# Kernel tuning notes

Measured on AMD Instinct MI355X. Metric: run time of the kernel, lower is better.

Reference implementation:

```python
import jax, jax.numpy as jnp
import numpy as np

PS = 4        # bkg_patch_size
PD = 1        # replicate pad
UFSTRIDE = 2  # patch-extraction stride
STRIDE = 1    # correlation stride
SCALE = 10.0  # softmax_scale


def pad_edge(x):
    return jnp.pad(x, ((0, 0), (0, 0), (PD, PD), (PD, PD)), mode='edge')


def unfold(x, ps, stride):
    # x: (B,C,H,W) -> (B, L, C, ps, ps), row-major over patch grid (matches F.unfold)
    B, C, H, W = x.shape
    oh = (H - ps) // stride + 1
    ow = (W - ps) // stride + 1
    ih = jnp.arange(oh)[:, None] * stride + jnp.arange(ps)[None, :]  # (oh, ps)
    iw = jnp.arange(ow)[:, None] * stride + jnp.arange(ps)[None, :]  # (ow, ps)
    p = x[:, :, ih][:, :, :, :, iw]            # (B,C,oh,ps,ow,ps)
    p = p.transpose(0, 2, 4, 1, 3, 5)          # (B,oh,ow,C,ps,ps)
    return p.reshape(B, oh * ow, C, ps, ps)


def diag3(x):
    # conv2d with 3x3 identity kernel, padding=1: out[i,j] = in[i-1,j-1]+in[i,j]+in[i+1,j+1]
    B, one, N, M = x.shape
    xp = jnp.pad(x, ((0, 0), (0, 0), (1, 1), (1, 1)))
    return xp[:, :, 0:N, 0:M] + xp[:, :, 1:N + 1, 1:M + 1] + xp[:, :, 2:N + 2, 2:M + 2]


def setup_inputs() -> dict:
    key = jax.random.key(0)
    k1, k2, k3 = jax.random.split(key, 3)
    B, C, H, W = 4, 64, 64, 64
    f = jax.random.normal(k1, (B, C, H, W), dtype=jnp.float32)
    b = jax.random.normal(k2, (B, C, H, W), dtype=jnp.float32)
    mask = (jax.random.uniform(k3, (B, 1, H, W)) < 0.25).astype(jnp.float32)
    return {"f": f, "b": b, "mask": mask}


def reference(f, b, mask):
    B, C, H, W = b.shape
    maskc = 1.0 - mask
    # --- get_conv_kernel: per-(batch,channel) L2-normalize b, extract patch kernels ---
    bn = b / jnp.sqrt(jnp.sum(b * b, axis=(2, 3), keepdims=True) + 1e-8)
    kernel = unfold(pad_edge(bn), PS, UFSTRIDE)                 # (B, L, C, ps, ps)
    mk = unfold(pad_edge(maskc), PS, UFSTRIDE)                  # (B, L, 1, ps, ps)
    mmk = jnp.mean(mk, axis=(2, 3, 4))[:, :, None, None]        # (B, L, 1, 1)
    L = kernel.shape[1]

    # --- batched grouped cross-correlation: conv f with per-sample patch kernels ---
    fpatch = unfold(pad_edge(f), PS, STRIDE)                    # (B, P, C, ps, ps)
    hs = (H + 2 * PD - PS) // STRIDE + 1
    ws = (W + 2 * PD - PS) // STRIDE + 1
    cos = jnp.einsum('bpcij,blcij->blp', fpatch, kernel)        # (B, L, P)
    cos = cos.reshape(B, L, hs, ws)

    # --- fuse: diagonal 3x3 convs along two axis pairings ---
    hb, wb = H // 2, W // 2
    cs = L
    c1 = diag3(cos.reshape(B, 1, cs, hs * ws))
    c1 = c1.reshape(B, 1, hb, wb, hs, ws).transpose(0, 1, 3, 2, 5, 4).reshape(B, 1, cs, hs * ws)
    c1 = diag3(c1)
    c1 = c1.reshape(B, 1, hb, wb, hs, ws).transpose(0, 1, 3, 2, 5, 4)
    cos = c1.reshape(B, cs, hs, ws)

    # --- irregular mask logic ---
    mp = unfold(pad_edge(maskc), PS, STRIDE)                    # (B, P, 1, ps, ps)
    mmp = jnp.mean(mp, axis=(2, 3, 4)).reshape(B, 1, hs, ws)    # (B, 1, hs, ws)
    mm = (mmk > mmp).astype(cos.dtype)                          # (B, L, hs, ws)
    ppp = (mmp > 0.5).astype(cos.dtype)
    mm = mm * ppp + (mmk == 1.0).astype(cos.dtype)
    mm = (mm > 0).astype(cos.dtype)

    cos = cos * mm
    return jax.nn.softmax(cos * SCALE, axis=1)
```

## Files before the change

### kernel.cpp

```cpp
#include <hip/hip_runtime.h>
#include <math.h>

#define NB 4
#define NC 64
#define NL 1024
#define NP 3969
#define PHW 63

typedef unsigned short ushort_t;
typedef __attribute__((ext_vector_type(8))) short short8;
typedef __attribute__((ext_vector_type(16))) float floatx16;

#define A_BSTRIDE 1048576
#define B_BSTRIDE 4194304

__global__ __launch_bounds__(256) void prep_kernel(const float* __restrict__ bsrc,
                                                   const float* __restrict__ mask,
                                                   float* __restrict__ invn,
                                                   float* __restrict__ mmk,
                                                   float* __restrict__ mmp,
                                                   ushort_t* __restrict__ Bhi,
                                                   ushort_t* __restrict__ Blo) {
    int blk = blockIdx.x;
    if (blk < 256) {
        const float* src = bsrc + (size_t)blk * 4096;
        float s = 0.f;
        for (int i = threadIdx.x; i < 4096; i += 256) { float v = src[i]; s += v * v; }
#pragma unroll
        for (int off = 32; off > 0; off >>= 1) s += __shfl_down(s, off, 64);
        __shared__ float part[4];
        if ((threadIdx.x & 63) == 0) part[threadIdx.x >> 6] = s;
        __syncthreads();
        if (threadIdx.x == 0) {
            float t = part[0] + part[1] + part[2] + part[3];
            invn[blk] = 1.0f / sqrtf(t + 1e-8f);
        }
    } else if (blk < 335) {
        int id = (blk - 256) * 256 + threadIdx.x;
        if (id < NB * NL) {
            int b = id >> 10, l = id & 1023;
            int lh = l >> 5, lw = l & 31;
            const float* m = mask + b * 4096;
            float s = 0.f;
#pragma unroll
            for (int i = 0; i < 4; ++i) {
                int r = min(max(2 * lh - 1 + i, 0), 63);
#pragma unroll
                for (int j = 0; j < 4; ++j) {
                    int c = min(max(2 * lw - 1 + j, 0), 63);
                    s += 1.0f - m[r * 64 + c];
                }
            }
            mmk[id] = s * (1.0f / 16.0f);
        } else {
            int id2 = id - NB * NL;
            if (id2 < NB * NP) {
                int b = id2 / NP, p = id2 - b * NP;
                int ph = p / PHW, pw = p - ph * PHW;
                const float* m = mask + b * 4096;
                float s = 0.f;
#pragma unroll
                for (int i = 0; i < 4; ++i) {
                    int r = min(max(ph - 1 + i, 0), 63);
#pragma unroll
                    for (int j = 0; j < 4; ++j) {
                        int c = min(max(pw - 1 + j, 0), 63);
                        s += 1.0f - m[r * 64 + c];
                    }
                }
                mmp[id2] = s * (1.0f / 16.0f);
            }
        }
    } else {
        int idx = (blk - 335) * 256 + threadIdx.x;
        int b = idx >> 15;
        int r = idx & 32767;
        int mat = r >> 14;
        int o = r & 16383;
        ushort_t* base = (mat ? Blo : Bhi) + (size_t)b * B_BSTRIDE + 124 * 32768;
        uint4 z = {0u, 0u, 0u, 0u};
        ((uint4*)base)[o] = z;
    }
}

__device__ inline void split_bf16(float v, ushort_t& hv, ushort_t& lv) {
    unsigned u = __float_as_uint(v);
    unsigned rr = u + 0x7FFFu + ((u >> 16) & 1u);
    hv = (ushort_t)(rr >> 16);
    float fh = __uint_as_float(((unsigned)hv) << 16);
    float remv = v - fh;
    unsigned u2 = __float_as_uint(remv);
    unsigned rr2 = u2 + 0x7FFFu + ((u2 >> 16) & 1u);
    lv = (ushort_t)(rr2 >> 16);
}

__device__ inline int frag_addr(int row, int kc) {
    return ((row >> 5) * 64 + kc) * 512 + (row & 31) * 8;
}

__global__ __launch_bounds__(256) void splitA_kernel(const float* __restrict__ bsrc,
                                                     const float* __restrict__ invn,
                                                     ushort_t* __restrict__ Ahi,
                                                     ushort_t* __restrict__ Alo) {
    __shared__ float fl[32 * 257];
    int lh = blockIdx.x, b = blockIdx.y, chalf = blockIdx.z;
    int t = threadIdx.x;
#pragma unroll
    for (int q = 0; q < 32; ++q) {
        int idx = t + (q << 8);
        int cl = idx >> 8, rem = idx & 255;
        int i = rem >> 6, s = rem & 63;
        int c = (chalf << 5) + cl;
        int r = min(max(2 * lh - 1 + i, 0), 63);
        fl[cl * 257 + rem] = bsrc[(((size_t)((b << 6) + c)) << 12) + (r << 6) + s];
    }
    __syncthreads();
    ushort_t* Ah = Ahi + (size_t)b * A_BSTRIDE;
    ushort_t* Al = Alo + (size_t)b * A_BSTRIDE;
#pragma unroll
    for (int q = 0; q < 4; ++q) {
        int pair = t + (q << 8);
        int lw = pair & 31, cl = pair >> 5;
        int c = (chalf << 5) + cl;
        float scale = invn[(b << 6) + c];
        const float* row = fl + cl * 257;
        __align__(16) ushort_t h[16];
        __align__(16) ushort_t lo[16];
#pragma unroll
        for (int i = 0; i < 4; ++i)
#pragma unroll
            for (int j = 0; j < 4; ++j) {
                int s = min(max(2 * lw - 1 + j, 0), 63);
                split_bf16(row[i * 64 + s] * scale, h[i * 4 + j], lo[i * 4 + j]);
            }
        int a = (lh * 64 + c) * 512 + lw * 8;
        *(uint4*)(Ah + a)       = *(uint4*)h;
        *(uint4*)(Ah + a + 256) = *(uint4*)(h + 8);
        *(uint4*)(Al + a)       = *(uint4*)lo;
        *(uint4*)(Al + a + 256) = *(uint4*)(lo + 8);
    }
}

__global__ __launch_bounds__(256) void splitB_kernel(const float* __restrict__ fsrc,
                                                     ushort_t* __restrict__ Bhi,
                                                     ushort_t* __restrict__ Blo) {
    __shared__ float fl[32 * 257];
    int ph = blockIdx.x, b = blockIdx.y, chalf = blockIdx.z;
    int t = threadIdx.x;
#pragma unroll
    for (int q = 0; q < 32; ++q) {
        int idx = t + (q << 8);
        int cl = idx >> 8, rem = idx & 255;
        int i = rem >> 6, s = rem & 63;
        int c = (chalf << 5) + cl;
        int r = min(max(ph - 1 + i, 0), 63);
        fl[cl * 257 + rem] = fsrc[(((size_t)((b << 6) + c)) << 12) + (r << 6) + s];
    }
    __syncthreads();
    ushort_t* Bh = Bhi + (size_t)b * B_BSTRIDE;
    ushort_t* Bl = Blo + (size_t)b * B_BSTRIDE;
#pragma unroll
    for (int q = 0; q < 8; ++q) {
        int pair = t + (q << 8);
        int pw = pair & 63, cl = pair >> 6;
        if (pw < PHW) {
            int c = (chalf << 5) + cl;
            const float* row = fl + cl * 257;
            __align__(16) ushort_t h[16];
            __align__(16) ushort_t lo[16];
#pragma unroll
            for (int i = 0; i < 4; ++i)
#pragma unroll
                for (int j = 0; j < 4; ++j) {
                    int s = min(max(pw - 1 + j, 0), 63);
                    split_bf16(row[i * 64 + s], h[i * 4 + j], lo[i * 4 + j]);
                }
            int p = ph * PHW + pw;
            int a = frag_addr(p, c);
            *(uint4*)(Bh + a)       = *(uint4*)h;
            *(uint4*)(Bh + a + 256) = *(uint4*)(h + 8);
            *(uint4*)(Bl + a)       = *(uint4*)lo;
            *(uint4*)(Bl + a + 256) = *(uint4*)(lo + 8);
        }
    }
}

__global__ __launch_bounds__(512, 2) void gemm_kernel(
    const ushort_t* __restrict__ Ahi, const ushort_t* __restrict__ Alo,
    const ushort_t* __restrict__ Bhi, const ushort_t* __restrict__ Blo,
    float* __restrict__ Rt) {
    __shared__ ushort_t smem[2][4][8][2][512];
    int tid = threadIdx.x;
    int lane = tid & 63, w = tid >> 6;
    int wl = w >> 2, wp = w & 3;
    int bid = blockIdx.x;
    int wid = ((bid & 7) << 5) + (bid >> 3);
    int b = wid >> 6;
    int bx = wid & 63;
    int L0 = (bx & 3) << 8;
    int P0 = (bx >> 2) << 8;

    int m = w >> 1;
    int rt0 = (w & 1) << 2;
    const ushort_t* gbase;
    if (m == 0)      gbase = Ahi + (size_t)b * A_BSTRIDE + (size_t)(L0 >> 5) * 32768;
    else if (m == 1) gbase = Alo + (size_t)b * A_BSTRIDE + (size_t)(L0 >> 5) * 32768;
    else if (m == 2) gbase = Bhi + (size_t)b * B_BSTRIDE + (size_t)(P0 >> 5) * 32768;
    else             gbase = Blo + (size_t)b * B_BSTRIDE + (size_t)(P0 >> 5) * 32768;
    gbase += (size_t)(lane << 3);
    int dst0 = ((((m << 3) + rt0) << 1)) * 512;

    ushort_t* buf0 = &smem[0][0][0][0][0];
    ushort_t* buf1 = &smem[1][0][0][0][0];

#define STAGE(dstp, t)                                                                     \
    do {                                                                                   \
        int kb = (t) << 1;                                                                 \
        _Pragma("unroll")                                                                  \
        for (int j = 0; j < 4; ++j)                                                        \
            _Pragma("unroll")                                                              \
            for (int ks = 0; ks < 2; ++ks)                                                 \
                __builtin_amdgcn_global_load_lds(                                          \
                    (const __attribute__((address_space(1))) void*)(                       \
                        gbase + (size_t)(rt0 + j) * 32768 + (size_t)(kb + ks) * 512),      \
                    (__attribute__((address_space(3))) void*)(                             \
                        (dstp) + dst0 + (((j << 1) + ks) * 512)),                          \
                    16, 0, 0);                                                             \
    } while (0)

    floatx16 acc[2][4];
#pragma unroll
    for (int i = 0; i < 2; ++i)
#pragma unroll
        for (int j = 0; j < 4; ++j)
#pragma unroll
            for (int r = 0; r < 16; ++r) acc[i][j][r] = 0.f;

    STAGE(buf0, 0);
    ushort_t* cur = buf0;
    ushort_t* nxt = buf1;

    int aoff = (wl << 2) * 1024;
    int boff = 16384 + (wp << 1) * 1024;

    for (int t = 0; t < 32; ++t) {
        asm volatile("" ::: "memory");
        __builtin_amdgcn_s_barrier();
        asm volatile("" ::: "memory");
        if (t < 31) {
            STAGE(nxt, t + 1);
            asm volatile("s_waitcnt vmcnt(8)" ::: "memory");
        } else {
            asm volatile("s_waitcnt vmcnt(0)" ::: "memory");
        }
        __builtin_amdgcn_s_barrier();
        asm volatile("" ::: "memory");

        const ushort_t* rb = cur + (lane << 3);
#pragma unroll
        for (int ks = 0; ks < 2; ++ks) {
            short8 ah[4], al[4], bh[2], bl[2];
#pragma unroll
            for (int lt = 0; lt < 4; ++lt) {
                ah[lt] = *(const short8*)(rb + aoff + lt * 1024 + ks * 512);
                al[lt] = *(const short8*)(rb + 8192 + aoff + lt * 1024 + ks * 512);
            }
#pragma unroll
            for (int pt = 0; pt < 2; ++pt) {
                bh[pt] = *(const short8*)(rb + boff + pt * 1024 + ks * 512);
                bl[pt] = *(const short8*)(rb + 8192 + boff + pt * 1024 + ks * 512);
            }
            __builtin_amdgcn_s_setprio(1);
#pragma unroll
            for (int pt = 0; pt < 2; ++pt)
#pragma unroll
                for (int lt = 0; lt < 4; ++lt) {
                    acc[pt][lt] = __builtin_amdgcn_mfma_f32_32x32x16_bf16(bh[pt], ah[lt], acc[pt][lt], 0, 0, 0);
                    acc[pt][lt] = __builtin_amdgcn_mfma_f32_32x32x16_bf16(bh[pt], al[lt], acc[pt][lt], 0, 0, 0);
                    acc[pt][lt] = __builtin_amdgcn_mfma_f32_32x32x16_bf16(bl[pt], ah[lt], acc[pt][lt], 0, 0, 0);
                }
            __builtin_amdgcn_s_setprio(0);
        }
        ushort_t* tmp = cur; cur = nxt; nxt = tmp;
    }
#undef STAGE

    int x = lane & 31, kg = lane >> 5;
    int pw0 = P0 + (wp << 6);
    int lw0 = L0 + (wl << 7);
#pragma unroll
    for (int pt = 0; pt < 2; ++pt)
#pragma unroll
        for (int lt = 0; lt < 4; ++lt)
#pragma unroll
            for (int r = 0; r < 16; ++r) {
                int p = pw0 + (pt << 5) + (r & 3) + ((r >> 2) << 3) + (kg << 2);
                int l = lw0 + (lt << 5) + x;
                if (p < NP) Rt[((size_t)b * NP + p) * NL + l] = acc[pt][lt][r];
            }
}

__global__ __launch_bounds__(256) void softmax_fused_kernel(const float* __restrict__ Rt,
                                                            const float* __restrict__ mmkA,
                                                            const float* __restrict__ mmpA,
                                                            float* __restrict__ E) {
    __shared__ float ld0[1024], ld1[1024], ld2[1024];
    __shared__ float red[8];
    int p = blockIdx.x, b = blockIdx.y;
    int ph = p / PHW, pw = p - ph * PHW;
    int t = threadIdx.x;
    int lane = t & 63, w = t >> 6;
    int l0 = t << 2;

    bool okm = (p != 0), okp = (p != 3968);
    int Pm = (ph > 0) ? p - 63 : 3905 + pw;
    int Pp = (ph < 62) ? p + 63 : pw + 1;

    const float* Rb = Rt + (size_t)b * NP * NL;
#define BUILD(dst, q)                                                   \
    do {                                                                \
        const float* base = Rb + (size_t)(q) * NL;                      \
        float4 r = *(const float4*)(base + l0);                         \
        if ((q) > 0) {                                                  \
            const float* pm = base - NL;                                \
            r.x += (l0 > 0) ? pm[l0 - 1] : 0.f;                         \
            r.y += pm[l0];  r.z += pm[l0 + 1];  r.w += pm[l0 + 2];      \
        }                                                               \
        if ((q) < NP - 1) {                                             \
            const float* pp = base + NL;                                \
            r.x += pp[l0 + 1];  r.y += pp[l0 + 2];  r.z += pp[l0 + 3];  \
            r.w += (l0 + 4 < NL) ? pp[l0 + 4] : 0.f;                    \
        }                                                               \
        *(float4*)(dst + l0) = r;                                       \
    } while (0)

    BUILD(ld0, p);
    if (okm) BUILD(ld1, Pm);
    if (okp) BUILD(ld2, Pp);
#undef BUILD
    __syncthreads();

    float4 vc = *(const float4*)(ld0 + l0);
    float4 vm = {0.f, 0.f, 0.f, 0.f}, vp = {0.f, 0.f, 0.f, 0.f};
    if (okm) {
        if (l0 >= 32) vm = *(const float4*)(ld1 + l0 - 32);
        else {
            vm.x = (l0 == 0) ? 0.f : ld1[l0 + 991];
            vm.y = ld1[l0 + 992];
            vm.z = ld1[l0 + 993];
            vm.w = ld1[l0 + 994];
        }
    }
    if (okp) {
        if (l0 < 992) vp = *(const float4*)(ld2 + l0 + 32);
        else {
            vp.x = ld2[l0 - 991];
            vp.y = ld2[l0 - 990];
            vp.z = ld2[l0 - 989];
            vp.w = (l0 + 3 == 1023) ? 0.f : ld2[l0 - 988];
        }
    }
    float mmpv = mmpA[b * NP + p];
    float4 km = *(const float4*)(mmkA + b * NL + l0);
    float lg[4];
    float fsum[4] = {vc.x + vm.x + vp.x, vc.y + vm.y + vp.y,
                     vc.z + vm.z + vp.z, vc.w + vm.w + vp.w};
    float kk[4] = {km.x, km.y, km.z, km.w};
#pragma unroll
    for (int i = 0; i < 4; ++i) {
        float mmv = (((kk[i] > mmpv) && (mmpv > 0.5f)) || (kk[i] == 1.0f)) ? 1.0f : 0.0f;
        lg[i] = fsum[i] * mmv * 10.0f;
    }
    float mx = fmaxf(fmaxf(lg[0], lg[1]), fmaxf(lg[2], lg[3]));
#pragma unroll
    for (int off = 32; off >= 1; off >>= 1) mx = fmaxf(mx, __shfl_xor(mx, off, 64));
    if (lane == 0) red[w] = mx;
    __syncthreads();
    mx = fmaxf(fmaxf(red[0], red[1]), fmaxf(red[2], red[3]));
    float e[4];
    float s = 0.f;
#pragma unroll
    for (int i = 0; i < 4; ++i) { e[i] = expf(lg[i] - mx); s += e[i]; }
#pragma unroll
    for (int off = 32; off >= 1; off >>= 1) s += __shfl_xor(s, off, 64);
    if (lane == 0) red[4 + w] = s;
    __syncthreads();
    float rinv = 1.0f / (red[4] + red[5] + red[6] + red[7]);
    float4 ev = {e[0] * rinv, e[1] * rinv, e[2] * rinv, e[3] * rinv};
    *(float4*)(E + (((size_t)b * NP + p) << 10) + l0) = ev;
}

__global__ __launch_bounds__(256) void transpose_kernel(const float* __restrict__ E,
                                                        float* __restrict__ out) {
    __shared__ float tile[63 * 65];
    int pt = blockIdx.x;
    int lt = blockIdx.y;
    int b  = blockIdx.z;
    int t = threadIdx.x;
    int p0 = pt * 63, l0 = lt << 6;
    const float* Eb = E + ((size_t)b * NP << 10);
    {
        int j = t & 63, i4 = t >> 6;
#pragma unroll
        for (int k = 0; k < 16; ++k) {
            int i = (k << 2) + i4;
            if (i < 63) tile[i * 65 + j] = Eb[((size_t)(p0 + i) << 10) + l0 + j];
        }
    }
    __syncthreads();
    {
        int ii = t & 63, jj4 = t >> 6;
        if (ii < 63) {
#pragma unroll
            for (int k = 0; k < 16; ++k) {
                int jj = (k << 2) + jj4;
                out[((size_t)b * NL + l0 + jj) * NP + p0 + ii] = tile[ii * 65 + jj];
            }
        }
    }
}

extern "C" void kernel_launch(void* const* d_in, const int* in_sizes, int n_in,
                              void* d_out, int out_size, void* d_ws, size_t ws_size,
                              hipStream_t stream) {
    const float* f    = (const float*)d_in[0];
    const float* b    = (const float*)d_in[1];
    const float* mask = (const float*)d_in[2];
    float* out = (float*)d_out;

    float* Rt = (float*)d_out;

    float* wsf = (float*)d_ws;
    float* E  = wsf + 16257024;
    ushort_t* Ahi = (ushort_t*)d_ws;
    ushort_t* Alo = Ahi + (size_t)NB * A_BSTRIDE;
    ushort_t* Bhi = Alo + (size_t)NB * A_BSTRIDE;
    ushort_t* Blo = Bhi + (size_t)NB * B_BSTRIDE;
    float* invn = wsf + 32514048;
    float* mmk = invn + 256;
    float* mmp = mmk + 4096;

    prep_kernel<<<dim3(847), dim3(256), 0, stream>>>(b, mask, invn, mmk, mmp, Bhi, Blo);
    splitA_kernel<<<dim3(32, 4, 2), dim3(256), 0, stream>>>(b, invn, Ahi, Alo);
    splitB_kernel<<<dim3(63, 4, 2), dim3(256), 0, stream>>>(f, Bhi, Blo);
    gemm_kernel<<<dim3(256), dim3(512), 0, stream>>>(Ahi, Alo, Bhi, Blo, Rt);
    softmax_fused_kernel<<<dim3(3969, 4), dim3(256), 0, stream>>>(Rt, mmk, mmp, E);
    transpose_kernel<<<dim3(63, 16, 4), dim3(256), 0, stream>>>(E, out);
}
```

Baseline: 265.2 us.

## Retile GEMM to 128x256 blocks of 4 waves with single-k-step stages

The split-bf16 GEMM now uses 512 blocks of 256 threads instead of 256 blocks of 512 threads. Each block covers 128 L by 256 P, stages one k-slice per iteration over 64 iterations, and each wave loads 6 segments. This doubles block count for better CU fill on the many-CU GPU and shrinks shared memory per block. The cost is more barriers per unit of work and lower A-tile reuse per block, which raises global and LDS traffic for A.

```diff
diff --git a/kernel.cpp b/kernel.cpp
--- a/kernel.cpp
+++ b/kernel.cpp
@@ -185,47 +185,47 @@
     }
 }
 
-__global__ __launch_bounds__(512, 2) void gemm_kernel(
+__global__ __launch_bounds__(256, 2) void gemm_kernel(
     const ushort_t* __restrict__ Ahi, const ushort_t* __restrict__ Alo,
     const ushort_t* __restrict__ Bhi, const ushort_t* __restrict__ Blo,
     float* __restrict__ Rt) {
-    __shared__ ushort_t smem[2][4][8][2][512];
+    __shared__ ushort_t smem[2][12288];
     int tid = threadIdx.x;
     int lane = tid & 63, w = tid >> 6;
-    int wl = w >> 2, wp = w & 3;
     int bid = blockIdx.x;
-    int wid = ((bid & 7) << 5) + (bid >> 3);
-    int b = wid >> 6;
-    int bx = wid & 63;
-    int L0 = (bx & 3) << 8;
-    int P0 = (bx >> 2) << 8;
-
-    int m = w >> 1;
-    int rt0 = (w & 1) << 2;
-    const ushort_t* gbase;
-    if (m == 0)      gbase = Ahi + (size_t)b * A_BSTRIDE + (size_t)(L0 >> 5) * 32768;
-    else if (m == 1) gbase = Alo + (size_t)b * A_BSTRIDE + (size_t)(L0 >> 5) * 32768;
-    else if (m == 2) gbase = Bhi + (size_t)b * B_BSTRIDE + (size_t)(P0 >> 5) * 32768;
-    else             gbase = Blo + (size_t)b * B_BSTRIDE + (size_t)(P0 >> 5) * 32768;
-    gbase += (size_t)(lane << 3);
-    int dst0 = ((((m << 3) + rt0) << 1)) * 512;
-
-    ushort_t* buf0 = &smem[0][0][0][0][0];
-    ushort_t* buf1 = &smem[1][0][0][0][0];
-
-#define STAGE(dstp, t)                                                                     \
+    int wid = ((bid & 7) << 6) + (bid >> 3);
+    int b = wid >> 7;
+    int rem = wid & 127;
+    int lg = rem >> 4;
+    int pg = rem & 15;
+    int L0 = lg << 7, P0 = pg << 8;
+
+    const ushort_t* segp[6];
+    int seg0 = w * 6;
+#pragma unroll
+    for (int i = 0; i < 6; ++i) {
+        int seg = seg0 + i;
+        const ushort_t* base;
+        int rt;
+        if (seg < 4)       { base = Ahi + (size_t)b * A_BSTRIDE + (size_t)(lg << 2) * 32768; rt = seg; }
+        else if (seg < 8)  { base = Alo + (size_t)b * A_BSTRIDE + (size_t)(lg << 2) * 32768; rt = seg - 4; }
+        else if (seg < 16) { base = Bhi + (size_t)b * B_BSTRIDE + (size_t)(pg << 3) * 32768; rt = seg - 8; }
+        else               { base = Blo + (size_t)b * B_BSTRIDE + (size_t)(pg << 3) * 32768; rt = seg - 16; }
+        segp[i] = base + (size_t)rt * 32768 + (size_t)(lane << 3);
+    }
+    int dst0 = seg0 * 512;
+
+    ushort_t* buf0 = smem[0];
+    ushort_t* buf1 = smem[1];
+
+#define STAGE(dstp, kc)                                                                    \
     do {                                                                                   \
-        int kb = (t) << 1;                                                                 \
         _Pragma("unroll")                                                                  \
-        for (int j = 0; j < 4; ++j)                                                        \
-            _Pragma("unroll")                                                              \
-            for (int ks = 0; ks < 2; ++ks)                                                 \
-                __builtin_amdgcn_global_load_lds(                                          \
-                    (const __attribute__((address_space(1))) void*)(                       \
-                        gbase + (size_t)(rt0 + j) * 32768 + (size_t)(kb + ks) * 512),      \
-                    (__attribute__((address_space(3))) void*)(                             \
-                        (dstp) + dst0 + (((j << 1) + ks) * 512)),                          \
-                    16, 0, 0);                                                             \
+        for (int i = 0; i < 6; ++i)                                                        \
+            __builtin_amdgcn_global_load_lds(                                              \
+                (const __attribute__((address_space(1))) void*)(segp[i] + (size_t)(kc) * 512), \
+                (__attribute__((address_space(3))) void*)((dstp) + dst0 + i * 512),        \
+                16, 0, 0);                                                                 \
     } while (0)
 
     floatx16 acc[2][4];
@@ -240,16 +240,15 @@
     ushort_t* cur = buf0;
     ushort_t* nxt = buf1;
 
-    int aoff = (wl << 2) * 1024;
-    int boff = 16384 + (wp << 1) * 1024;
-
-    for (int t = 0; t < 32; ++t) {
+    int boff0 = 4096 + (w << 1) * 512;
+
+    for (int t = 0; t < 64; ++t) {
         asm volatile("" ::: "memory");
         __builtin_amdgcn_s_barrier();
         asm volatile("" ::: "memory");
-        if (t < 31) {
+        if (t < 63) {
             STAGE(nxt, t + 1);
-            asm volatile("s_waitcnt vmcnt(8)" ::: "memory");
+            asm volatile("s_waitcnt vmcnt(6)" ::: "memory");
         } else {
             asm volatile("s_waitcnt vmcnt(0)" ::: "memory");
         }
@@ -257,37 +256,33 @@
         asm volatile("" ::: "memory");
 
         const ushort_t* rb = cur + (lane << 3);
-#pragma unroll
-        for (int ks = 0; ks < 2; ++ks) {
-            short8 ah[4], al[4], bh[2], bl[2];
+        short8 ah[4], al[4], bh[2], bl[2];
+#pragma unroll
+        for (int lt = 0; lt < 4; ++lt) {
+            ah[lt] = *(const short8*)(rb + lt * 512);
+            al[lt] = *(const short8*)(rb + 2048 + lt * 512);
+        }
+#pragma unroll
+        for (int pt = 0; pt < 2; ++pt) {
+            bh[pt] = *(const short8*)(rb + boff0 + pt * 512);
+            bl[pt] = *(const short8*)(rb + 4096 + boff0 + pt * 512);
+        }
+        __builtin_amdgcn_s_setprio(1);
+#pragma unroll
+        for (int pt = 0; pt < 2; ++pt)
 #pragma unroll
             for (int lt = 0; lt < 4; ++lt) {
-                ah[lt] = *(const short8*)(rb + aoff + lt * 1024 + ks * 512);
-                al[lt] = *(const short8*)(rb + 8192 + aoff + lt * 1024 + ks * 512);
-            }
-#pragma unroll
-            for (int pt = 0; pt < 2; ++pt) {
-                bh[pt] = *(const short8*)(rb + boff + pt * 1024 + ks * 512);
-                bl[pt] = *(const short8*)(rb + 8192 + boff + pt * 1024 + ks * 512);
-            }
-            __builtin_amdgcn_s_setprio(1);
-#pragma unroll
-            for (int pt = 0; pt < 2; ++pt)
-#pragma unroll
-                for (int lt = 0; lt < 4; ++lt) {
-                    acc[pt][lt] = __builtin_amdgcn_mfma_f32_32x32x16_bf16(bh[pt], ah[lt], acc[pt][lt], 0, 0, 0);
-                    acc[pt][lt] = __builtin_amdgcn_mfma_f32_32x32x16_bf16(bh[pt], al[lt], acc[pt][lt], 0, 0, 0);
-                    acc[pt][lt] = __builtin_amdgcn_mfma_f32_32x32x16_bf16(bl[pt], ah[lt], acc[pt][lt], 0, 0, 0);
-                }
-            __builtin_amdgcn_s_setprio(0);
-        }
+                acc[pt][lt] = __builtin_amdgcn_mfma_f32_32x32x16_bf16(bh[pt], ah[lt], acc[pt][lt], 0, 0, 0);
+                acc[pt][lt] = __builtin_amdgcn_mfma_f32_32x32x16_bf16(bh[pt], al[lt], acc[pt][lt], 0, 0, 0);
+                acc[pt][lt] = __builtin_amdgcn_mfma_f32_32x32x16_bf16(bl[pt], ah[lt], acc[pt][lt], 0, 0, 0);
+            }
+        __builtin_amdgcn_s_setprio(0);
         ushort_t* tmp = cur; cur = nxt; nxt = tmp;
     }
 #undef STAGE
 
     int x = lane & 31, kg = lane >> 5;
-    int pw0 = P0 + (wp << 6);
-    int lw0 = L0 + (wl << 7);
+    int pw0 = P0 + (w << 6);
 #pragma unroll
     for (int pt = 0; pt < 2; ++pt)
 #pragma unroll
@@ -295,7 +290,7 @@
 #pragma unroll
             for (int r = 0; r < 16; ++r) {
                 int p = pw0 + (pt << 5) + (r & 3) + ((r >> 2) << 3) + (kg << 2);
-                int l = lw0 + (lt << 5) + x;
+                int l = L0 + (lt << 5) + x;
                 if (p < NP) Rt[((size_t)b * NP + p) * NL + l] = acc[pt][lt][r];
             }
 }
@@ -443,7 +438,7 @@
     prep_kernel<<<dim3(847), dim3(256), 0, stream>>>(b, mask, invn, mmk, mmp, Bhi, Blo);
     splitA_kernel<<<dim3(32, 4, 2), dim3(256), 0, stream>>>(b, invn, Ahi, Alo);
     splitB_kernel<<<dim3(63, 4, 2), dim3(256), 0, stream>>>(f, Bhi, Blo);
-    gemm_kernel<<<dim3(256), dim3(512), 0, stream>>>(Ahi, Alo, Bhi, Blo, Rt);
+    gemm_kernel<<<dim3(512), dim3(256), 0, stream>>>(Ahi, Alo, Bhi, Blo, Rt);
     softmax_fused_kernel<<<dim3(3969, 4), dim3(256), 0, stream>>>(Rt, mmk, mmp, E);
     transpose_kernel<<<dim3(63, 16, 4), dim3(256), 0, stream>>>(E, out);
 }
```

After: 267.8 us. About the same (+1.0%).
